# Kernel optimization log

Hardware: AMD Instinct MI355X
Metric: run time of the kernel (lower is better)

Reference implementation:

```python
import jax, jax.numpy as jnp
import numpy as np

N_TOKEN = 267735
HEAD = 20000
CUTOFFS = [20000, 20008, 20016, 200000, 267735]  # from cl_root_leaf_dict with 2 roots of 8 leaves
N_ROOTS = 2


def setup_inputs() -> dict:
    key = jax.random.key(0)
    k1, k2, k3, k4 = jax.random.split(key, 4)
    N, D = 1024, 1024
    hidden = jax.random.normal(k1, (N, D), dtype=jnp.float32)
    target = jax.random.randint(k2, (N,), 0, N_TOKEN)
    W = jax.random.normal(k3, (N_TOKEN, D), dtype=jnp.float32) * 0.02
    b = jnp.zeros((N_TOKEN,), dtype=jnp.float32)
    cluster_weight = jax.random.normal(k4, (2, D), dtype=jnp.float32) * 0.02
    cluster_bias = jnp.zeros((2,), dtype=jnp.float32)
    return {"hidden": hidden, "target": target, "W": W, "b": b,
            "cluster_weight": cluster_weight, "cluster_bias": cluster_bias}


def _nll(hidden, target, W, b, cw, cb):
    cutoff_ends = [0] + CUTOFFS
    # head = first 20000 vocab rows + 2 cluster rows (d_proj == d_embed -> no projection)
    head_w = jnp.concatenate([W[:HEAD], cw], axis=0)          # [20002, D]
    head_b = jnp.concatenate([b[:HEAD], cb], axis=0)          # [20002]
    head_lp = jax.nn.log_softmax(hidden @ head_w.T + head_b, axis=-1)  # [N, 20002]
    n_head_cols = head_lp.shape[1]
    rows = jnp.arange(hidden.shape[0])
    # segment 0: target in [0, 20000) -> nll directly from head log-probs
    lp0 = head_lp[rows, jnp.clip(target, 0, HEAD - 1)]
    nll = -lp0  # only valid where target < HEAD; overwritten below otherwise
    for i in range(1, len(CUTOFFS)):
        l, r = cutoff_ends[i], cutoff_ends[i + 1]
        # per-segment tail logits for all tokens (masked combine keeps shapes static)
        tail_lp = jax.nn.log_softmax(hidden @ W[l:r].T + b[l:r], axis=-1)  # [N, r-l]
        # routing column exactly as in the torch code:
        # j = i-1 for root segments, -(i - n_roots) for the two cluster segments
        j = (i - 1) if i <= N_ROOTS else (n_head_cols - (i - N_ROOTS))
        lp_i = head_lp[:, j] + tail_lp[rows, jnp.clip(target - l, 0, r - l - 1)]
        mask = (target >= l) & (target < r)
        nll = jnp.where(mask, -lp_i, nll)
    return nll


def reference(hidden, target, W, b, cluster_weight, cluster_bias):
    return _nll(hidden, target, W, b, cluster_weight, cluster_bias)
```

## Files before the change

### kernel.cpp

```cpp
#include <hip/hip_runtime.h>
#include <hip/hip_bf16.h>

#define D_DIM 1024
#define NTOK 267735
#define NEXT_ 267737
#define HEADN 20000

typedef __attribute__((ext_vector_type(8))) short bf16x8;
typedef __attribute__((ext_vector_type(4))) float f32x4;

__device__ __forceinline__ int seg_of(int c){
  if (c < HEADN)  return 0;
  if (c < 20008)  return 1;
  if (c < 20016)  return 2;
  if (c < 200000) return 3;
  if (c < NTOK)   return 4;
  return 0;
}

__device__ __forceinline__ unsigned pack2(float x, float y){
  __hip_bfloat16 a = __float2bfloat16(x);
  __hip_bfloat16 b = __float2bfloat16(y);
  unsigned short ua = *reinterpret_cast<unsigned short*>(&a);
  unsigned short ub = *reinterpret_cast<unsigned short*>(&b);
  return (unsigned)ua | ((unsigned)ub << 16);
}

#define BM 512
#define BN 128
#define BK 32
#define NTHREADS 1024
#define KSTEPS (D_DIM/BK)
#define NROWB 2
#define NCOLT 2092
#define NBLK 4192

#define APRIME_OFF 32768
#define APRIME_BYTES (1024*1024*2)

__device__ __forceinline__ int swz_w(int r, int k4){
  int c = (k4 >> 1) ^ ((r >> 1) & 3);
  return r*32 + c*8 + (k4 & 1)*4;
}
__device__ __forceinline__ int swz_r(int row, int q){
  return row*32 + ((q ^ ((row >> 1) & 3)) << 3);
}

__global__ void prep_convert(const float* __restrict__ hidden,
                             unsigned short* __restrict__ Ap)
{
  int t = blockIdx.x * blockDim.x + threadIdx.x;
  int r16 = t & 15, kc = (t >> 4) & 127, rb = t >> 11;
  const float4* src = reinterpret_cast<const float4*>(hidden + ((size_t)(rb*16 + r16) * D_DIM + kc*8));
  float4 x = src[0], y = src[1];
  uint4 o;
  o.x = pack2(x.x, x.y); o.y = pack2(x.z, x.w);
  o.z = pack2(y.x, y.y); o.w = pack2(y.z, y.w);
  reinterpret_cast<uint4*>(Ap)[t] = o;
}

__global__ __launch_bounds__(NTHREADS, 1) void gemm_lse_adir(
    const unsigned short* __restrict__ Ap, const float* __restrict__ W,
    const float* __restrict__ bias,   const float* __restrict__ cw,
    const float* __restrict__ cb,     float* __restrict__ accg)
{
  const int b = blockIdx.x;
  const int k8 = b & 7;
  const int sq_ = b >> 3;
  const int xb = sq_ & 1;
  const int yb = (sq_ >> 1) * 8 + k8;
  if (yb >= NCOLT) return;

  __shared__ unsigned short lsB0[BN * 32];
  __shared__ unsigned short lsB1[BN * 32];

  const int tid = threadIdx.x;
  const int rowBase = xb * BM;
  const int colBase = yb * BN;

  const float* bSrc; int bRow, bK4;
  {
    bRow = tid >> 3; bK4 = tid & 7;
    int c = colBase + bRow;
    const float* base;
    if (c < NTOK)       base = W  + (size_t)c * D_DIM;
    else if (c < NEXT_) base = cw + (size_t)(c - NTOK) * D_DIM;
    else                base = W;
    bSrc = base + bK4*4;
  }

  const int lane = tid & 63;
  const int wv = tid >> 6;
  const int wm = wv >> 1;
  const int wn = wv & 1;
  const int q  = lane >> 4;
  const int r16 = lane & 15;

  const int wB0 = swz_w(bRow, bK4);
  const int rB0 = swz_r(wn*64 +  0 + r16, q), rB1 = swz_r(wn*64 + 16 + r16, q);
  const int rB2 = swz_r(wn*64 + 32 + r16, q), rB3 = swz_r(wn*64 + 48 + r16, q);

  const unsigned short* a0 = Ap + (size_t)(xb*32 + wm*4 + 0)*16384 + q*128 + r16*8;
  const unsigned short* a1 = Ap + (size_t)(xb*32 + wm*4 + 1)*16384 + q*128 + r16*8;
  const unsigned short* a2 = Ap + (size_t)(xb*32 + wm*4 + 2)*16384 + q*128 + r16*8;
  const unsigned short* a3 = Ap + (size_t)(xb*32 + wm*4 + 3)*16384 + q*128 + r16*8;

  f32x4 acc[4][4];
#pragma unroll
  for (int i=0;i<4;++i)
#pragma unroll
    for (int j=0;j<4;++j) acc[i][j] = (f32x4){0.f,0.f,0.f,0.f};

  {
    float4 v0 = *reinterpret_cast<const float4*>(bSrc);
    unsigned* p = reinterpret_cast<unsigned*>(&lsB0[wB0]);
    p[0] = pack2(v0.x, v0.y); p[1] = pack2(v0.z, v0.w);
  }
  __syncthreads();

  for (int kt = 0; kt < KSTEPS; ++kt){
    unsigned short* Lr = (kt & 1) ? lsB1 : lsB0;
    unsigned short* Lw = (kt & 1) ? lsB0 : lsB1;
    const bool havenext = (kt + 1 < KSTEPS);

    float4 nb0;
    if (havenext) nb0 = *reinterpret_cast<const float4*>(bSrc + (kt+1)*BK);

    bf16x8 af0 = *reinterpret_cast<const bf16x8*>(a0 + kt*512);
    bf16x8 af1 = *reinterpret_cast<const bf16x8*>(a1 + kt*512);
    bf16x8 af2 = *reinterpret_cast<const bf16x8*>(a2 + kt*512);
    bf16x8 af3 = *reinterpret_cast<const bf16x8*>(a3 + kt*512);

    bf16x8 bf0 = *reinterpret_cast<const bf16x8*>(&Lr[rB0]);
    bf16x8 bf1 = *reinterpret_cast<const bf16x8*>(&Lr[rB1]);
    bf16x8 bf2 = *reinterpret_cast<const bf16x8*>(&Lr[rB2]);
    bf16x8 bf3 = *reinterpret_cast<const bf16x8*>(&Lr[rB3]);

    acc[0][0] = __builtin_amdgcn_mfma_f32_16x16x32_bf16(af0, bf0, acc[0][0], 0,0,0);
    acc[0][1] = __builtin_amdgcn_mfma_f32_16x16x32_bf16(af0, bf1, acc[0][1], 0,0,0);
    acc[0][2] = __builtin_amdgcn_mfma_f32_16x16x32_bf16(af0, bf2, acc[0][2], 0,0,0);
    acc[0][3] = __builtin_amdgcn_mfma_f32_16x16x32_bf16(af0, bf3, acc[0][3], 0,0,0);
    acc[1][0] = __builtin_amdgcn_mfma_f32_16x16x32_bf16(af1, bf0, acc[1][0], 0,0,0);
    acc[1][1] = __builtin_amdgcn_mfma_f32_16x16x32_bf16(af1, bf1, acc[1][1], 0,0,0);
    acc[1][2] = __builtin_amdgcn_mfma_f32_16x16x32_bf16(af1, bf2, acc[1][2], 0,0,0);
    acc[1][3] = __builtin_amdgcn_mfma_f32_16x16x32_bf16(af1, bf3, acc[1][3], 0,0,0);
    acc[2][0] = __builtin_amdgcn_mfma_f32_16x16x32_bf16(af2, bf0, acc[2][0], 0,0,0);
    acc[2][1] = __builtin_amdgcn_mfma_f32_16x16x32_bf16(af2, bf1, acc[2][1], 0,0,0);
    acc[2][2] = __builtin_amdgcn_mfma_f32_16x16x32_bf16(af2, bf2, acc[2][2], 0,0,0);
    acc[2][3] = __builtin_amdgcn_mfma_f32_16x16x32_bf16(af2, bf3, acc[2][3], 0,0,0);
    acc[3][0] = __builtin_amdgcn_mfma_f32_16x16x32_bf16(af3, bf0, acc[3][0], 0,0,0);
    acc[3][1] = __builtin_amdgcn_mfma_f32_16x16x32_bf16(af3, bf1, acc[3][1], 0,0,0);
    acc[3][2] = __builtin_amdgcn_mfma_f32_16x16x32_bf16(af3, bf2, acc[3][2], 0,0,0);
    acc[3][3] = __builtin_amdgcn_mfma_f32_16x16x32_bf16(af3, bf3, acc[3][3], 0,0,0);

    if (havenext){
      unsigned* p = reinterpret_cast<unsigned*>(&Lw[wB0]);
      p[0] = pack2(nb0.x, nb0.y); p[1] = pack2(nb0.z, nb0.w);
    }
    __syncthreads();
  }

  int sq[4]; float bq[4];
#pragma unroll
  for (int f=0; f<4; ++f){
    int c = colBase + wn*64 + f*16 + r16;
    if (c < NTOK)       { sq[f] = seg_of(c); bq[f] = bias[c]; }
    else if (c < NEXT_) { sq[f] = 0;         bq[f] = cb[c - NTOK]; }
    else                { sq[f] = -1;        bq[f] = 0.f; }
  }
  int sfirst = seg_of(colBase);
  int clast  = colBase + BN - 1; if (clast > NEXT_-1) clast = NEXT_-1;
  int slast  = seg_of(clast);
  int smin = sfirst, smax = slast;
  if (slast < sfirst){ smin = 0; smax = 4; }

#pragma unroll
  for (int i=0;i<4;++i){
#pragma unroll
    for (int r=0;r<4;++r){
      float e[4];
#pragma unroll
      for (int f=0;f<4;++f) e[f] = __expf(acc[i][f][r] + bq[f]);
      int rowg = rowBase + wm*64 + i*16 + (lane>>4)*4 + r;
      for (int s2 = smin; s2 <= smax; ++s2){
        float p = 0.f;
#pragma unroll
        for (int f=0;f<4;++f) p += (sq[f]==s2) ? e[f] : 0.f;
#pragma unroll
        for (int off=1; off<16; off<<=1) p += __shfl_xor(p, off, 16);
        if ((lane & 15) == 0 && p != 0.f) atomicAdd(&accg[rowg*8 + s2], p);
      }
    }
  }
}

__global__ __launch_bounds__(256) void finalize_kernel(
    const float* __restrict__ hidden, const int* __restrict__ target,
    const float* __restrict__ W,      const float* __restrict__ bias,
    const float* __restrict__ cw,     const float* __restrict__ cb,
    const float* __restrict__ accg,   float* __restrict__ out)
{
  const int row  = blockIdx.x * 4 + (threadIdx.x >> 6);
  const int lane = threadIdx.x & 63;
  const int t = target[row];

  const float4* h4 = reinterpret_cast<const float4*>(hidden + (size_t)row * D_DIM);
  const float4* w1 = reinterpret_cast<const float4*>(W + (size_t)t * D_DIM);
  int s = 0; const float* jraw = W; float jb = 0.f;
  if (t >= HEADN){
    if      (t < 20008)  { s=1; jraw = W;          jb = bias[0]; }
    else if (t < 20016)  { s=2; jraw = W + D_DIM;  jb = bias[1]; }
    else if (t < 200000) { s=3; jraw = cw + D_DIM; jb = cb[1];   }
    else                 { s=4; jraw = cw;         jb = cb[0];   }
  }
  const float4* w2 = reinterpret_cast<const float4*>(jraw);

  float p1 = 0.f, p2 = 0.f;
#pragma unroll
  for (int j=0;j<4;++j){
    float4 hv = h4[lane + 64*j];
    float4 av = w1[lane + 64*j];
    float4 bv = w2[lane + 64*j];
    p1 += hv.x*av.x + hv.y*av.y + hv.z*av.z + hv.w*av.w;
    p2 += hv.x*bv.x + hv.y*bv.y + hv.z*bv.z + hv.w*bv.w;
  }
#pragma unroll
  for (int off=32; off; off>>=1){
    p1 += __shfl_xor(p1, off, 64);
    p2 += __shfl_xor(p2, off, 64);
  }

  if (lane == 0){
    float lseH = __logf(accg[row*8 + 0]);
    float nll;
    if (t < HEADN){
      nll = -(p1 + bias[t] - lseH);
    } else {
      float lseS = __logf(accg[row*8 + s]);
      nll = -((p2 + jb - lseH) + (p1 + bias[t] - lseS));
    }
    out[row] = nll;
  }
}

extern "C" void kernel_launch(void* const* d_in, const int* in_sizes, int n_in,
                              void* d_out, int out_size, void* d_ws, size_t ws_size,
                              hipStream_t stream)
{
  const float* hidden = (const float*)d_in[0];
  const int*   target = (const int*)  d_in[1];
  const float* W      = (const float*)d_in[2];
  const float* bias   = (const float*)d_in[3];
  const float* cw     = (const float*)d_in[4];
  const float* cb     = (const float*)d_in[5];
  float* out  = (float*)d_out;
  float* accg = (float*)d_ws;
  unsigned short* Ap = (unsigned short*)((char*)d_ws + APRIME_OFF);

  hipMemsetAsync(accg, 0, 1024*8*sizeof(float), stream);

  prep_convert<<<512, 256, 0, stream>>>(hidden, Ap);
  gemm_lse_adir<<<NBLK, NTHREADS, 0, stream>>>(Ap, W, bias, cw, cb, accg);
  finalize_kernel<<<256, 256, 0, stream>>>(hidden, target, W, bias, cw, cb, accg, out);
}
```

Baseline: 943.1 us.

## Halve GEMM row tile, register double-buffer A fragments, lighter barrier

```diff
diff --git a/kernel.cpp b/kernel.cpp
--- a/kernel.cpp
+++ b/kernel.cpp
@@ -26,17 +26,19 @@
   return (unsigned)ua | ((unsigned)ub << 16);
 }
 
-#define BM 512
+#define BM 256
 #define BN 128
 #define BK 32
-#define NTHREADS 1024
+#define NTHREADS 512
 #define KSTEPS (D_DIM/BK)
-#define NROWB 2
 #define NCOLT 2092
-#define NBLK 4192
+#define NBLK 8384
 
 #define APRIME_OFF 32768
 #define APRIME_BYTES (1024*1024*2)
+
+#define BAR() do{ asm volatile("s_waitcnt lgkmcnt(0)" ::: "memory"); \
+                  __builtin_amdgcn_s_barrier(); }while(0)
 
 __device__ __forceinline__ int swz_w(int r, int k4){
   int c = (k4 >> 1) ^ ((r >> 1) & 3);
@@ -67,8 +69,8 @@
   const int b = blockIdx.x;
   const int k8 = b & 7;
   const int sq_ = b >> 3;
-  const int xb = sq_ & 1;
-  const int yb = (sq_ >> 1) * 8 + k8;
+  const int xb = sq_ & 3;
+  const int yb = (sq_ >> 2) * 8 + k8;
   if (yb >= NCOLT) return;
 
   __shared__ unsigned short lsB0[BN * 32];
@@ -78,15 +80,24 @@
   const int rowBase = xb * BM;
   const int colBase = yb * BN;
 
-  const float* bSrc; int bRow, bK4;
+  const float* bSrc0; const float* bSrc1; int bRow0, bRow1, bK40, bK41;
   {
-    bRow = tid >> 3; bK4 = tid & 7;
-    int c = colBase + bRow;
+    int idx = tid;            bRow0 = idx >> 3; bK40 = idx & 7;
+    int c = colBase + bRow0;
     const float* base;
     if (c < NTOK)       base = W  + (size_t)c * D_DIM;
     else if (c < NEXT_) base = cw + (size_t)(c - NTOK) * D_DIM;
     else                base = W;
-    bSrc = base + bK4*4;
+    bSrc0 = base + bK40*4;
+  }
+  {
+    int idx = tid + NTHREADS; bRow1 = idx >> 3; bK41 = idx & 7;
+    int c = colBase + bRow1;
+    const float* base;
+    if (c < NTOK)       base = W  + (size_t)c * D_DIM;
+    else if (c < NEXT_) base = cw + (size_t)(c - NTOK) * D_DIM;
+    else                base = W;
+    bSrc1 = base + bK41*4;
   }
 
   const int lane = tid & 63;
@@ -96,14 +107,14 @@
   const int q  = lane >> 4;
   const int r16 = lane & 15;
 
-  const int wB0 = swz_w(bRow, bK4);
+  const int wB0 = swz_w(bRow0, bK40), wB1 = swz_w(bRow1, bK41);
   const int rB0 = swz_r(wn*64 +  0 + r16, q), rB1 = swz_r(wn*64 + 16 + r16, q);
   const int rB2 = swz_r(wn*64 + 32 + r16, q), rB3 = swz_r(wn*64 + 48 + r16, q);
 
-  const unsigned short* a0 = Ap + (size_t)(xb*32 + wm*4 + 0)*16384 + q*128 + r16*8;
-  const unsigned short* a1 = Ap + (size_t)(xb*32 + wm*4 + 1)*16384 + q*128 + r16*8;
-  const unsigned short* a2 = Ap + (size_t)(xb*32 + wm*4 + 2)*16384 + q*128 + r16*8;
-  const unsigned short* a3 = Ap + (size_t)(xb*32 + wm*4 + 3)*16384 + q*128 + r16*8;
+  const unsigned short* a0 = Ap + (size_t)(xb*16 + wm*4 + 0)*16384 + q*128 + r16*8;
+  const unsigned short* a1 = Ap + (size_t)(xb*16 + wm*4 + 1)*16384 + q*128 + r16*8;
+  const unsigned short* a2 = Ap + (size_t)(xb*16 + wm*4 + 2)*16384 + q*128 + r16*8;
+  const unsigned short* a3 = Ap + (size_t)(xb*16 + wm*4 + 3)*16384 + q*128 + r16*8;
 
   f32x4 acc[4][4];
 #pragma unroll
@@ -111,53 +122,78 @@
 #pragma unroll
     for (int j=0;j<4;++j) acc[i][j] = (f32x4){0.f,0.f,0.f,0.f};
 
+  bf16x8 xA0, xA1, xA2, xA3;
+  bf16x8 yA0, yA1, yA2, yA3;
+
+#define LOAD_AX(kn) \
+    xA0 = *reinterpret_cast<const bf16x8*>(a0 + (kn)*512); \
+    xA1 = *reinterpret_cast<const bf16x8*>(a1 + (kn)*512); \
+    xA2 = *reinterpret_cast<const bf16x8*>(a2 + (kn)*512); \
+    xA3 = *reinterpret_cast<const bf16x8*>(a3 + (kn)*512);
+#define LOAD_AY(kn) \
+    yA0 = *reinterpret_cast<const bf16x8*>(a0 + (kn)*512); \
+    yA1 = *reinterpret_cast<const bf16x8*>(a1 + (kn)*512); \
+    yA2 = *reinterpret_cast<const bf16x8*>(a2 + (kn)*512); \
+    yA3 = *reinterpret_cast<const bf16x8*>(a3 + (kn)*512);
+
+#define MFMA16(A0,A1,A2,A3,L) { \
+    bf16x8 bf0 = *reinterpret_cast<const bf16x8*>(&L[rB0]); \
+    bf16x8 bf1 = *reinterpret_cast<const bf16x8*>(&L[rB1]); \
+    bf16x8 bf2 = *reinterpret_cast<const bf16x8*>(&L[rB2]); \
+    bf16x8 bf3 = *reinterpret_cast<const bf16x8*>(&L[rB3]); \
+    acc[0][0] = __builtin_amdgcn_mfma_f32_16x16x32_bf16(A0, bf0, acc[0][0], 0,0,0); \
+    acc[0][1] = __builtin_amdgcn_mfma_f32_16x16x32_bf16(A0, bf1, acc[0][1], 0,0,0); \
+    acc[0][2] = __builtin_amdgcn_mfma_f32_16x16x32_bf16(A0, bf2, acc[0][2], 0,0,0); \
+    acc[0][3] = __builtin_amdgcn_mfma_f32_16x16x32_bf16(A0, bf3, acc[0][3], 0,0,0); \
+    acc[1][0] = __builtin_amdgcn_mfma_f32_16x16x32_bf16(A1, bf0, acc[1][0], 0,0,0); \
+    acc[1][1] = __builtin_amdgcn_mfma_f32_16x16x32_bf16(A1, bf1, acc[1][1], 0,0,0); \
+    acc[1][2] = __builtin_amdgcn_mfma_f32_16x16x32_bf16(A1, bf2, acc[1][2], 0,0,0); \
+    acc[1][3] = __builtin_amdgcn_mfma_f32_16x16x32_bf16(A1, bf3, acc[1][3], 0,0,0); \
+    acc[2][0] = __builtin_amdgcn_mfma_f32_16x16x32_bf16(A2, bf0, acc[2][0], 0,0,0); \
+    acc[2][1] = __builtin_amdgcn_mfma_f32_16x16x32_bf16(A2, bf1, acc[2][1], 0,0,0); \
+    acc[2][2] = __builtin_amdgcn_mfma_f32_16x16x32_bf16(A2, bf2, acc[2][2], 0,0,0); \
+    acc[2][3] = __builtin_amdgcn_mfma_f32_16x16x32_bf16(A2, bf3, acc[2][3], 0,0,0); \
+    acc[3][0] = __builtin_amdgcn_mfma_f32_16x16x32_bf16(A3, bf0, acc[3][0], 0,0,0); \
+    acc[3][1] = __builtin_amdgcn_mfma_f32_16x16x32_bf16(A3, bf1, acc[3][1], 0,0,0); \
+    acc[3][2] = __builtin_amdgcn_mfma_f32_16x16x32_bf16(A3, bf2, acc[3][2], 0,0,0); \
+    acc[3][3] = __builtin_amdgcn_mfma_f32_16x16x32_bf16(A3, bf3, acc[3][3], 0,0,0); }
+
+#define WRITE_B(L, v0, v1) { \
+    unsigned* p; \
+    p = reinterpret_cast<unsigned*>(&L[wB0]); p[0] = pack2(v0.x, v0.y); p[1] = pack2(v0.z, v0.w); \
+    p = reinterpret_cast<unsigned*>(&L[wB1]); p[0] = pack2(v1.x, v1.y); p[1] = pack2(v1.z, v1.w); }
+
+  LOAD_AX(0);
   {
-    float4 v0 = *reinterpret_cast<const float4*>(bSrc);
-    unsigned* p = reinterpret_cast<unsigned*>(&lsB0[wB0]);
-    p[0] = pack2(v0.x, v0.y); p[1] = pack2(v0.z, v0.w);
-  }
-  __syncthreads();
-
-  for (int kt = 0; kt < KSTEPS; ++kt){
-    unsigned short* Lr = (kt & 1) ? lsB1 : lsB0;
-    unsigned short* Lw = (kt & 1) ? lsB0 : lsB1;
-    const bool havenext = (kt + 1 < KSTEPS);
-
-    float4 nb0;
-    if (havenext) nb0 = *reinterpret_cast<const float4*>(bSrc + (kt+1)*BK);
-
-    bf16x8 af0 = *reinterpret_cast<const bf16x8*>(a0 + kt*512);
-    bf16x8 af1 = *reinterpret_cast<const bf16x8*>(a1 + kt*512);
-    bf16x8 af2 = *reinterpret_cast<const bf16x8*>(a2 + kt*512);
-    bf16x8 af3 = *reinterpret_cast<const bf16x8*>(a3 + kt*512);
-
-    bf16x8 bf0 = *reinterpret_cast<const bf16x8*>(&Lr[rB0]);
-    bf16x8 bf1 = *reinterpret_cast<const bf16x8*>(&Lr[rB1]);
-    bf16x8 bf2 = *reinterpret_cast<const bf16x8*>(&Lr[rB2]);
-    bf16x8 bf3 = *reinterpret_cast<const bf16x8*>(&Lr[rB3]);
-
-    acc[0][0] = __builtin_amdgcn_mfma_f32_16x16x32_bf16(af0, bf0, acc[0][0], 0,0,0);
-    acc[0][1] = __builtin_amdgcn_mfma_f32_16x16x32_bf16(af0, bf1, acc[0][1], 0,0,0);
-    acc[0][2] = __builtin_amdgcn_mfma_f32_16x16x32_bf16(af0, bf2, acc[0][2], 0,0,0);
-    acc[0][3] = __builtin_amdgcn_mfma_f32_16x16x32_bf16(af0, bf3, acc[0][3], 0,0,0);
-    acc[1][0] = __builtin_amdgcn_mfma_f32_16x16x32_bf16(af1, bf0, acc[1][0], 0,0,0);
-    acc[1][1] = __builtin_amdgcn_mfma_f32_16x16x32_bf16(af1, bf1, acc[1][1], 0,0,0);
-    acc[1][2] = __builtin_amdgcn_mfma_f32_16x16x32_bf16(af1, bf2, acc[1][2], 0,0,0);
-    acc[1][3] = __builtin_amdgcn_mfma_f32_16x16x32_bf16(af1, bf3, acc[1][3], 0,0,0);
-    acc[2][0] = __builtin_amdgcn_mfma_f32_16x16x32_bf16(af2, bf0, acc[2][0], 0,0,0);
-    acc[2][1] = __builtin_amdgcn_mfma_f32_16x16x32_bf16(af2, bf1, acc[2][1], 0,0,0);
-    acc[2][2] = __builtin_amdgcn_mfma_f32_16x16x32_bf16(af2, bf2, acc[2][2], 0,0,0);
-    acc[2][3] = __builtin_amdgcn_mfma_f32_16x16x32_bf16(af2, bf3, acc[2][3], 0,0,0);
-    acc[3][0] = __builtin_amdgcn_mfma_f32_16x16x32_bf16(af3, bf0, acc[3][0], 0,0,0);
-    acc[3][1] = __builtin_amdgcn_mfma_f32_16x16x32_bf16(af3, bf1, acc[3][1], 0,0,0);
-    acc[3][2] = __builtin_amdgcn_mfma_f32_16x16x32_bf16(af3, bf2, acc[3][2], 0,0,0);
-    acc[3][3] = __builtin_amdgcn_mfma_f32_16x16x32_bf16(af3, bf3, acc[3][3], 0,0,0);
-
-    if (havenext){
-      unsigned* p = reinterpret_cast<unsigned*>(&Lw[wB0]);
-      p[0] = pack2(nb0.x, nb0.y); p[1] = pack2(nb0.z, nb0.w);
+    float4 v0 = *reinterpret_cast<const float4*>(bSrc0);
+    float4 v1 = *reinterpret_cast<const float4*>(bSrc1);
+    WRITE_B(lsB0, v0, v1);
+  }
+  BAR();
+
+  for (int kt2 = 0; kt2 < KSTEPS/2; ++kt2){
+    {
+      const int kn = 2*kt2 + 1;
+      float4 nb0 = *reinterpret_cast<const float4*>(bSrc0 + kn*BK);
+      float4 nb1 = *reinterpret_cast<const float4*>(bSrc1 + kn*BK);
+      LOAD_AY(kn);
+      MFMA16(xA0, xA1, xA2, xA3, lsB0);
+      WRITE_B(lsB1, nb0, nb1);
+      BAR();
     }
-    __syncthreads();
+    {
+      const int kn = 2*kt2 + 2;
+      if (kn < KSTEPS){
+        float4 nb0 = *reinterpret_cast<const float4*>(bSrc0 + kn*BK);
+        float4 nb1 = *reinterpret_cast<const float4*>(bSrc1 + kn*BK);
+        LOAD_AX(kn);
+        MFMA16(yA0, yA1, yA2, yA3, lsB1);
+        WRITE_B(lsB0, nb0, nb1);
+        BAR();
+      } else {
+        MFMA16(yA0, yA1, yA2, yA3, lsB1);
+      }
+    }
   }
 
   int sq[4]; float bq[4];
```

Result: slower. 1.275 ms (+35.2%).

## Stage W tiles via direct global-to-LDS loads in fp32 and halve block rows

Applied to the files above, without the earlier changes.

```diff
diff --git a/kernel.cpp b/kernel.cpp
--- a/kernel.cpp
+++ b/kernel.cpp
@@ -8,6 +8,7 @@
 
 typedef __attribute__((ext_vector_type(8))) short bf16x8;
 typedef __attribute__((ext_vector_type(4))) float f32x4;
+typedef __attribute__((ext_vector_type(4))) unsigned uint4v;
 
 __device__ __forceinline__ int seg_of(int c){
   if (c < HEADN)  return 0;
@@ -26,24 +27,21 @@
   return (unsigned)ua | ((unsigned)ub << 16);
 }
 
-#define BM 512
+#define BM 256
 #define BN 128
 #define BK 32
-#define NTHREADS 1024
+#define NTHREADS 512
 #define KSTEPS (D_DIM/BK)
-#define NROWB 2
 #define NCOLT 2092
-#define NBLK 4192
+#define NBLK 8384
 
 #define APRIME_OFF 32768
 #define APRIME_BYTES (1024*1024*2)
 
-__device__ __forceinline__ int swz_w(int r, int k4){
-  int c = (k4 >> 1) ^ ((r >> 1) & 3);
-  return r*32 + c*8 + (k4 & 1)*4;
-}
-__device__ __forceinline__ int swz_r(int row, int q){
-  return row*32 + ((q ^ ((row >> 1) & 3)) << 3);
+__device__ __forceinline__ void stage16(const float* g, unsigned short* l){
+  __builtin_amdgcn_global_load_lds(
+      (const __attribute__((address_space(1))) void*)g,
+      (__attribute__((address_space(3))) void*)l, 16, 0, 0);
 }
 
 __global__ void prep_convert(const float* __restrict__ hidden,
@@ -67,27 +65,16 @@
   const int b = blockIdx.x;
   const int k8 = b & 7;
   const int sq_ = b >> 3;
-  const int xb = sq_ & 1;
-  const int yb = (sq_ >> 1) * 8 + k8;
+  const int xb = sq_ & 3;
+  const int yb = (sq_ >> 2) * 8 + k8;
   if (yb >= NCOLT) return;
 
-  __shared__ unsigned short lsB0[BN * 32];
-  __shared__ unsigned short lsB1[BN * 32];
+  __shared__ unsigned short lsB0[BN * 64];
+  __shared__ unsigned short lsB1[BN * 64];
 
   const int tid = threadIdx.x;
   const int rowBase = xb * BM;
   const int colBase = yb * BN;
-
-  const float* bSrc; int bRow, bK4;
-  {
-    bRow = tid >> 3; bK4 = tid & 7;
-    int c = colBase + bRow;
-    const float* base;
-    if (c < NTOK)       base = W  + (size_t)c * D_DIM;
-    else if (c < NEXT_) base = cw + (size_t)(c - NTOK) * D_DIM;
-    else                base = W;
-    bSrc = base + bK4*4;
-  }
 
   const int lane = tid & 63;
   const int wv = tid >> 6;
@@ -96,14 +83,40 @@
   const int q  = lane >> 4;
   const int r16 = lane & 15;
 
-  const int wB0 = swz_w(bRow, bK4);
-  const int rB0 = swz_r(wn*64 +  0 + r16, q), rB1 = swz_r(wn*64 + 16 + r16, q);
-  const int rB2 = swz_r(wn*64 + 32 + r16, q), rB3 = swz_r(wn*64 + 48 + r16, q);
-
-  const unsigned short* a0 = Ap + (size_t)(xb*32 + wm*4 + 0)*16384 + q*128 + r16*8;
-  const unsigned short* a1 = Ap + (size_t)(xb*32 + wm*4 + 1)*16384 + q*128 + r16*8;
-  const unsigned short* a2 = Ap + (size_t)(xb*32 + wm*4 + 2)*16384 + q*128 + r16*8;
-  const unsigned short* a3 = Ap + (size_t)(xb*32 + wm*4 + 3)*16384 + q*128 + r16*8;
+  const float* sp0; const float* sp1;
+  {
+    int f = tid;        int row = f >> 3; int kc = (f & 7) ^ (row & 7);
+    int c = colBase + row;
+    const float* base = (c < NTOK)  ? (W  + (size_t)c * D_DIM)
+                      : (c < NEXT_) ? (cw + (size_t)(c - NTOK) * D_DIM) : W;
+    sp0 = base + kc*4;
+  }
+  {
+    int f = 512 + tid;  int row = f >> 3; int kc = (f & 7) ^ (row & 7);
+    int c = colBase + row;
+    const float* base = (c < NTOK)  ? (W  + (size_t)c * D_DIM)
+                      : (c < NEXT_) ? (cw + (size_t)(c - NTOK) * D_DIM) : W;
+    sp1 = base + kc*4;
+  }
+  const int dst0 = wv*512;
+  const int dst1 = 4096 + wv*512;
+
+#define STAGE(Lbuf, kn) do{ \
+    stage16(sp0 + (kn)*BK, &Lbuf[dst0]); \
+    stage16(sp1 + (kn)*BK, &Lbuf[dst1]); }while(0)
+
+  int loO[4], hiO[4];
+#pragma unroll
+  for (int j=0;j<4;++j){
+    int row = wn*64 + j*16 + r16;
+    loO[j] = row*64 + (((2*q  ) ^ (row & 7)) << 3);
+    hiO[j] = row*64 + (((2*q+1) ^ (row & 7)) << 3);
+  }
+
+  const unsigned short* a0 = Ap + (size_t)(xb*16 + wm*4 + 0)*16384 + q*128 + r16*8;
+  const unsigned short* a1 = Ap + (size_t)(xb*16 + wm*4 + 1)*16384 + q*128 + r16*8;
+  const unsigned short* a2 = Ap + (size_t)(xb*16 + wm*4 + 2)*16384 + q*128 + r16*8;
+  const unsigned short* a3 = Ap + (size_t)(xb*16 + wm*4 + 3)*16384 + q*128 + r16*8;
 
   f32x4 acc[4][4];
 #pragma unroll
@@ -111,52 +124,48 @@
 #pragma unroll
     for (int j=0;j<4;++j) acc[i][j] = (f32x4){0.f,0.f,0.f,0.f};
 
-  {
-    float4 v0 = *reinterpret_cast<const float4*>(bSrc);
-    unsigned* p = reinterpret_cast<unsigned*>(&lsB0[wB0]);
-    p[0] = pack2(v0.x, v0.y); p[1] = pack2(v0.z, v0.w);
-  }
+#define BFRAG(Lr, j, out) { \
+    float4 lo = *reinterpret_cast<const float4*>(&Lr[loO[j]]); \
+    float4 hi = *reinterpret_cast<const float4*>(&Lr[hiO[j]]); \
+    uint4v uu; \
+    uu.x = pack2(lo.x, lo.y); uu.y = pack2(lo.z, lo.w); \
+    uu.z = pack2(hi.x, hi.y); uu.w = pack2(hi.z, hi.w); \
+    out = __builtin_bit_cast(bf16x8, uu); }
+
+  STAGE(lsB0, 0);
   __syncthreads();
 
   for (int kt = 0; kt < KSTEPS; ++kt){
     unsigned short* Lr = (kt & 1) ? lsB1 : lsB0;
     unsigned short* Lw = (kt & 1) ? lsB0 : lsB1;
-    const bool havenext = (kt + 1 < KSTEPS);
-
-    float4 nb0;
-    if (havenext) nb0 = *reinterpret_cast<const float4*>(bSrc + (kt+1)*BK);
 
     bf16x8 af0 = *reinterpret_cast<const bf16x8*>(a0 + kt*512);
     bf16x8 af1 = *reinterpret_cast<const bf16x8*>(a1 + kt*512);
     bf16x8 af2 = *reinterpret_cast<const bf16x8*>(a2 + kt*512);
     bf16x8 af3 = *reinterpret_cast<const bf16x8*>(a3 + kt*512);
 
-    bf16x8 bf0 = *reinterpret_cast<const bf16x8*>(&Lr[rB0]);
-    bf16x8 bf1 = *reinterpret_cast<const bf16x8*>(&Lr[rB1]);
-    bf16x8 bf2 = *reinterpret_cast<const bf16x8*>(&Lr[rB2]);
-    bf16x8 bf3 = *reinterpret_cast<const bf16x8*>(&Lr[rB3]);
-
-    acc[0][0] = __builtin_amdgcn_mfma_f32_16x16x32_bf16(af0, bf0, acc[0][0], 0,0,0);
-    acc[0][1] = __builtin_amdgcn_mfma_f32_16x16x32_bf16(af0, bf1, acc[0][1], 0,0,0);
-    acc[0][2] = __builtin_amdgcn_mfma_f32_16x16x32_bf16(af0, bf2, acc[0][2], 0,0,0);
-    acc[0][3] = __builtin_amdgcn_mfma_f32_16x16x32_bf16(af0, bf3, acc[0][3], 0,0,0);
-    acc[1][0] = __builtin_amdgcn_mfma_f32_16x16x32_bf16(af1, bf0, acc[1][0], 0,0,0);
-    acc[1][1] = __builtin_amdgcn_mfma_f32_16x16x32_bf16(af1, bf1, acc[1][1], 0,0,0);
-    acc[1][2] = __builtin_amdgcn_mfma_f32_16x16x32_bf16(af1, bf2, acc[1][2], 0,0,0);
-    acc[1][3] = __builtin_amdgcn_mfma_f32_16x16x32_bf16(af1, bf3, acc[1][3], 0,0,0);
-    acc[2][0] = __builtin_amdgcn_mfma_f32_16x16x32_bf16(af2, bf0, acc[2][0], 0,0,0);
-    acc[2][1] = __builtin_amdgcn_mfma_f32_16x16x32_bf16(af2, bf1, acc[2][1], 0,0,0);
-    acc[2][2] = __builtin_amdgcn_mfma_f32_16x16x32_bf16(af2, bf2, acc[2][2], 0,0,0);
-    acc[2][3] = __builtin_amdgcn_mfma_f32_16x16x32_bf16(af2, bf3, acc[2][3], 0,0,0);
-    acc[3][0] = __builtin_amdgcn_mfma_f32_16x16x32_bf16(af3, bf0, acc[3][0], 0,0,0);
-    acc[3][1] = __builtin_amdgcn_mfma_f32_16x16x32_bf16(af3, bf1, acc[3][1], 0,0,0);
-    acc[3][2] = __builtin_amdgcn_mfma_f32_16x16x32_bf16(af3, bf2, acc[3][2], 0,0,0);
-    acc[3][3] = __builtin_amdgcn_mfma_f32_16x16x32_bf16(af3, bf3, acc[3][3], 0,0,0);
-
-    if (havenext){
-      unsigned* p = reinterpret_cast<unsigned*>(&Lw[wB0]);
-      p[0] = pack2(nb0.x, nb0.y); p[1] = pack2(nb0.z, nb0.w);
-    }
+    if (kt + 1 < KSTEPS) STAGE(Lw, kt+1);
+
+    bf16x8 b0, b1, b2, b3;
+    BFRAG(Lr, 0, b0); BFRAG(Lr, 1, b1); BFRAG(Lr, 2, b2); BFRAG(Lr, 3, b3);
+
+    acc[0][0] = __builtin_amdgcn_mfma_f32_16x16x32_bf16(af0, b0, acc[0][0], 0,0,0);
+    acc[0][1] = __builtin_amdgcn_mfma_f32_16x16x32_bf16(af0, b1, acc[0][1], 0,0,0);
+    acc[0][2] = __builtin_amdgcn_mfma_f32_16x16x32_bf16(af0, b2, acc[0][2], 0,0,0);
+    acc[0][3] = __builtin_amdgcn_mfma_f32_16x16x32_bf16(af0, b3, acc[0][3], 0,0,0);
+    acc[1][0] = __builtin_amdgcn_mfma_f32_16x16x32_bf16(af1, b0, acc[1][0], 0,0,0);
+    acc[1][1] = __builtin_amdgcn_mfma_f32_16x16x32_bf16(af1, b1, acc[1][1], 0,0,0);
+    acc[1][2] = __builtin_amdgcn_mfma_f32_16x16x32_bf16(af1, b2, acc[1][2], 0,0,0);
+    acc[1][3] = __builtin_amdgcn_mfma_f32_16x16x32_bf16(af1, b3, acc[1][3], 0,0,0);
+    acc[2][0] = __builtin_amdgcn_mfma_f32_16x16x32_bf16(af2, b0, acc[2][0], 0,0,0);
+    acc[2][1] = __builtin_amdgcn_mfma_f32_16x16x32_bf16(af2, b1, acc[2][1], 0,0,0);
+    acc[2][2] = __builtin_amdgcn_mfma_f32_16x16x32_bf16(af2, b2, acc[2][2], 0,0,0);
+    acc[2][3] = __builtin_amdgcn_mfma_f32_16x16x32_bf16(af2, b3, acc[2][3], 0,0,0);
+    acc[3][0] = __builtin_amdgcn_mfma_f32_16x16x32_bf16(af3, b0, acc[3][0], 0,0,0);
+    acc[3][1] = __builtin_amdgcn_mfma_f32_16x16x32_bf16(af3, b1, acc[3][1], 0,0,0);
+    acc[3][2] = __builtin_amdgcn_mfma_f32_16x16x32_bf16(af3, b2, acc[3][2], 0,0,0);
+    acc[3][3] = __builtin_amdgcn_mfma_f32_16x16x32_bf16(af3, b3, acc[3][3], 0,0,0);
+
     __syncthreads();
   }
 
```

Measured after the change: 887.5 us. 5.9% less time.
